# Kernel optimization log

Measured on AMD Instinct MI355X. Metric: run time of the kernel, lower is better.

The kernel has to match this reference:

```python
import jax, jax.numpy as jnp
import numpy as np

DT = 0.01
STEPS = 30
D = 2048


def setup_inputs() -> dict:
    key = jax.random.key(0)
    ks = jax.random.split(key, 7)
    B, S = 4, 4096
    x = jax.random.normal(ks[0], (B, S, D), jnp.float32)
    lorenz = jnp.array([10.0, 28.0, 8.0 / 3.0], jnp.float32)
    strength = jnp.float32(0.3)
    W_in = jax.random.normal(ks[1], (3, D), jnp.float32) / np.sqrt(D)
    b_in = jax.random.normal(ks[2], (3,), jnp.float32) * 0.01
    W_out = jax.random.normal(ks[3], (D, 18), jnp.float32) / np.sqrt(18.0)
    b_out = jax.random.normal(ks[4], (D,), jnp.float32) * 0.01
    return {"x": x, "lorenz": lorenz, "strength": strength,
            "W_in": W_in, "b_in": b_in, "W_out": W_out, "b_out": b_out}


def _deriv(s, sigma, rho, beta):
    xx, yy, zz = s[..., 0], s[..., 1], s[..., 2]
    return jnp.stack([sigma * (yy - xx), xx * (rho - zz) - yy, xx * yy - beta * zz], axis=-1)


def reference(x, lorenz, strength, W_in, b_in, W_out, b_out):
    orig_shape = x.shape
    xf = x.reshape(-1, x.shape[-1])            # [N, D]
    state0 = xf @ W_in.T + b_in                # [N, 3]
    params = jnp.clip(jnp.abs(lorenz), 0.1, None)
    sigma, rho, beta = params[0], params[1], params[2]

    def step(s, _):
        k1 = _deriv(s, sigma, rho, beta)
        k2 = _deriv(s + 0.5 * DT * k1, sigma, rho, beta)
        k3 = _deriv(s + 0.5 * DT * k2, sigma, rho, beta)
        k4 = _deriv(s + DT * k3, sigma, rho, beta)
        s2 = s + (DT / 6.0) * (k1 + 2.0 * k2 + 2.0 * k3 + k4)
        return s2, s2

    _, ys = jax.lax.scan(step, state0, None, length=STEPS)  # [STEPS, N, 3]
    traj = jnp.concatenate([state0[:, None], jnp.moveaxis(ys, 0, 1)], axis=1)  # [N, STEPS+1, 3]

    feats = jnp.concatenate([
        traj[:, 0],                         # initial state
        traj[:, -1],                        # final state
        traj.mean(axis=1),
        traj.std(axis=1, ddof=1),           # torch.std is unbiased by default
        traj.min(axis=1),
        traj.max(axis=1),
    ], axis=-1)                             # [N, 18]

    pert = feats @ W_out.T + b_out          # [N, D]
    out = xf + jnp.tanh(pert) * jnp.abs(strength)
    return out.reshape(orig_shape)
```

## Files before the change

### kernel.cpp

```cpp
#include <hip/hip_runtime.h>
#include <math.h>

#define DD 2048
#define DTC 0.01f
#define NSTEPS 30

__device__ __forceinline__ void lorenz_deriv(float x, float y, float z,
                                             float sigma, float rho, float beta,
                                             float& dx, float& dy, float& dz) {
    dx = sigma * (y - x);
    dy = x * (rho - z) - y;
    dz = x * y - beta * z;
}

__device__ __forceinline__ float fast_tanh(float p) {
    float e = __expf(2.0f * p);
    return 1.0f - __fdividef(2.0f, e + 1.0f);
}

__global__ __launch_bounds__(256) void k1_feats(
    const float* __restrict__ x, const float* __restrict__ lorenz,
    const float* __restrict__ W_in, const float* __restrict__ b_in,
    float* __restrict__ feats) {
    const int tid = threadIdx.x;
    const int row0 = blockIdx.x * 8;
    const int d0 = tid * 8;

    float w0[8], w1[8], w2[8];
    {
        const float4* p0 = reinterpret_cast<const float4*>(W_in + 0 * DD + d0);
        const float4* p1 = reinterpret_cast<const float4*>(W_in + 1 * DD + d0);
        const float4* p2 = reinterpret_cast<const float4*>(W_in + 2 * DD + d0);
        float4 a, b;
        a = p0[0]; b = p0[1];
        w0[0]=a.x; w0[1]=a.y; w0[2]=a.z; w0[3]=a.w; w0[4]=b.x; w0[5]=b.y; w0[6]=b.z; w0[7]=b.w;
        a = p1[0]; b = p1[1];
        w1[0]=a.x; w1[1]=a.y; w1[2]=a.z; w1[3]=a.w; w1[4]=b.x; w1[5]=b.y; w1[6]=b.z; w1[7]=b.w;
        a = p2[0]; b = p2[1];
        w2[0]=a.x; w2[1]=a.y; w2[2]=a.z; w2[3]=a.w; w2[4]=b.x; w2[5]=b.y; w2[6]=b.z; w2[7]=b.w;
    }

    float part[8][3];
#pragma unroll
    for (int r = 0; r < 8; ++r) {
        const float4* p = reinterpret_cast<const float4*>(x + (size_t)(row0 + r) * DD + d0);
        float4 a = p[0], b = p[1];
        float xv[8] = {a.x, a.y, a.z, a.w, b.x, b.y, b.z, b.w};
        float s0 = 0.f, s1 = 0.f, s2 = 0.f;
#pragma unroll
        for (int j = 0; j < 8; ++j) {
            s0 += xv[j] * w0[j];
            s1 += xv[j] * w1[j];
            s2 += xv[j] * w2[j];
        }
        part[r][0] = s0; part[r][1] = s1; part[r][2] = s2;
    }

    __shared__ float red[4][24];
    __shared__ float st0[8][3];
    const int lane = tid & 63;
    const int wv = tid >> 6;
#pragma unroll
    for (int r = 0; r < 8; ++r) {
#pragma unroll
        for (int k = 0; k < 3; ++k) {
            float v = part[r][k];
#pragma unroll
            for (int off = 32; off > 0; off >>= 1) v += __shfl_xor(v, off, 64);
            if (lane == 0) red[wv][r * 3 + k] = v;
        }
    }
    __syncthreads();
    if (tid < 24) {
        float v = red[0][tid] + red[1][tid] + red[2][tid] + red[3][tid] + b_in[tid % 3];
        st0[tid / 3][tid % 3] = v;
    }
    __syncthreads();

    if (tid < 8) {
        const float sigma = fmaxf(fabsf(lorenz[0]), 0.1f);
        const float rho   = fmaxf(fabsf(lorenz[1]), 0.1f);
        const float beta  = fmaxf(fabsf(lorenz[2]), 0.1f);
        float sx = st0[tid][0], sy = st0[tid][1], sz = st0[tid][2];
        const float ix = sx, iy = sy, iz = sz;
        float sux = sx, suy = sy, suz = sz;
        float sqx = sx * sx, sqy = sy * sy, sqz = sz * sz;
        float mnx = sx, mny = sy, mnz = sz;
        float mxx = sx, mxy = sy, mxz = sz;
#pragma unroll 1
        for (int t = 0; t < NSTEPS; ++t) {
            float k1x, k1y, k1z, k2x, k2y, k2z, k3x, k3y, k3z, k4x, k4y, k4z;
            float ax, ay, az;
            lorenz_deriv(sx, sy, sz, sigma, rho, beta, k1x, k1y, k1z);
            ax = sx + 0.5f * DTC * k1x; ay = sy + 0.5f * DTC * k1y; az = sz + 0.5f * DTC * k1z;
            lorenz_deriv(ax, ay, az, sigma, rho, beta, k2x, k2y, k2z);
            ax = sx + 0.5f * DTC * k2x; ay = sy + 0.5f * DTC * k2y; az = sz + 0.5f * DTC * k2z;
            lorenz_deriv(ax, ay, az, sigma, rho, beta, k3x, k3y, k3z);
            ax = sx + DTC * k3x; ay = sy + DTC * k3y; az = sz + DTC * k3z;
            lorenz_deriv(ax, ay, az, sigma, rho, beta, k4x, k4y, k4z);
            sx += (DTC / 6.0f) * (k1x + 2.0f * k2x + 2.0f * k3x + k4x);
            sy += (DTC / 6.0f) * (k1y + 2.0f * k2y + 2.0f * k3y + k4y);
            sz += (DTC / 6.0f) * (k1z + 2.0f * k2z + 2.0f * k3z + k4z);
            sux += sx; suy += sy; suz += sz;
            sqx += sx * sx; sqy += sy * sy; sqz += sz * sz;
            mnx = fminf(mnx, sx); mny = fminf(mny, sy); mnz = fminf(mnz, sz);
            mxx = fmaxf(mxx, sx); mxy = fmaxf(mxy, sy); mxz = fmaxf(mxz, sz);
        }
        const float inv31 = 1.0f / 31.0f;
        const float inv30 = 1.0f / 30.0f;
        const float mex = sux * inv31, mey = suy * inv31, mez = suz * inv31;
        const float vax = fmaxf((sqx - sux * mex) * inv30, 0.0f);
        const float vay = fmaxf((sqy - suy * mey) * inv30, 0.0f);
        const float vaz = fmaxf((sqz - suz * mez) * inv30, 0.0f);
        float* f = feats + (size_t)(row0 + tid) * 18;
        f[0]  = ix;  f[1]  = iy;  f[2]  = iz;
        f[3]  = sx;  f[4]  = sy;  f[5]  = sz;
        f[6]  = mex; f[7]  = mey; f[8]  = mez;
        f[9]  = sqrtf(vax); f[10] = sqrtf(vay); f[11] = sqrtf(vaz);
        f[12] = mnx; f[13] = mny; f[14] = mnz;
        f[15] = mxx; f[16] = mxy; f[17] = mxz;
    }
}

__global__ __launch_bounds__(256) void k2_out(
    const float* __restrict__ x, const float* __restrict__ feats,
    const float* __restrict__ W_out, const float* __restrict__ b_out,
    const float* __restrict__ strength, float* __restrict__ out) {
    const int tid = threadIdx.x;
    const int row0 = blockIdx.x * 32;
    const int j0 = blockIdx.y * 512 + tid * 2;

    float w0[18], w1[18];
    {
        const float* wp = W_out + (size_t)j0 * 18;
#pragma unroll
        for (int k = 0; k < 18; ++k) { w0[k] = wp[k]; w1[k] = wp[18 + k]; }
    }
    const float2 bo = *reinterpret_cast<const float2*>(b_out + j0);
    const float sabs = fabsf(strength[0]);

#pragma unroll 1
    for (int r = 0; r < 32; ++r) {
        const int row = row0 + r;
        const float* f = feats + (size_t)row * 18;
        float p0 = bo.x, p1 = bo.y;
#pragma unroll
        for (int k = 0; k < 18; ++k) {
            const float fk = f[k];
            p0 += fk * w0[k];
            p1 += fk * w1[k];
        }
        const float2 xv = *reinterpret_cast<const float2*>(x + (size_t)row * DD + j0);
        float2 o;
        o.x = xv.x + fast_tanh(p0) * sabs;
        o.y = xv.y + fast_tanh(p1) * sabs;
        *reinterpret_cast<float2*>(out + (size_t)row * DD + j0) = o;
    }
}

extern "C" void kernel_launch(void* const* d_in, const int* in_sizes, int n_in,
                              void* d_out, int out_size, void* d_ws, size_t ws_size,
                              hipStream_t stream) {
    const float* x        = (const float*)d_in[0];
    const float* lorenz   = (const float*)d_in[1];
    const float* strength = (const float*)d_in[2];
    const float* W_in     = (const float*)d_in[3];
    const float* b_in     = (const float*)d_in[4];
    const float* W_out    = (const float*)d_in[5];
    const float* b_out    = (const float*)d_in[6];
    float* out   = (float*)d_out;
    float* feats = (float*)d_ws;

    const int N = in_sizes[0] / DD;

    k1_feats<<<N / 8, 256, 0, stream>>>(x, lorenz, W_in, b_in, feats);

    dim3 g2(N / 32, DD / 512);
    k2_out<<<g2, 256, 0, stream>>>(x, feats, W_out, b_out, strength, out);
}
```

Baseline: 87.03 us.

## Fuse feature and output kernels with x tile staged in LDS

Merges the two kernels into one that loads a 4-row tile of x into LDS with global_load_lds, computes the projection, the RK4 trajectory and the features, then produces the output rows from the same LDS tile. This avoids reading x twice from HBM, the feats round trip through global memory, and the second launch. In exchange each block uses 32KB of LDS, which limits occupancy. W_out is now reloaded per block (2048x18 floats) with a strided, uncoalesced access, and the serial 30-step RK4 runs on only 4 threads while the rest of the block waits.

```diff
diff --git a/kernel.cpp b/kernel.cpp
--- a/kernel.cpp
+++ b/kernel.cpp
@@ -4,6 +4,7 @@
 #define DD 2048
 #define DTC 0.01f
 #define NSTEPS 30
+#define ROWS 4
 
 __device__ __forceinline__ void lorenz_deriv(float x, float y, float z,
                                              float sigma, float rho, float beta,
@@ -18,12 +19,20 @@
     return 1.0f - __fdividef(2.0f, e + 1.0f);
 }
 
-__global__ __launch_bounds__(256) void k1_feats(
+__global__ __launch_bounds__(256) void fused_enrich(
     const float* __restrict__ x, const float* __restrict__ lorenz,
     const float* __restrict__ W_in, const float* __restrict__ b_in,
-    float* __restrict__ feats) {
+    const float* __restrict__ W_out, const float* __restrict__ b_out,
+    const float* __restrict__ strength, float* __restrict__ out) {
+    __shared__ float x_tile[ROWS * DD];
+    __shared__ float red[4][ROWS * 3];
+    __shared__ float st0[ROWS][3];
+    __shared__ float feats_lds[ROWS][20];
+
     const int tid = threadIdx.x;
-    const int row0 = blockIdx.x * 8;
+    const int lane = tid & 63;
+    const int wv = tid >> 6;
+    const int row0 = blockIdx.x * ROWS;
     const int d0 = tid * 8;
 
     float w0[8], w1[8], w2[8];
@@ -40,10 +49,23 @@
         w2[0]=a.x; w2[1]=a.y; w2[2]=a.z; w2[3]=a.w; w2[4]=b.x; w2[5]=b.y; w2[6]=b.z; w2[7]=b.w;
     }
 
-    float part[8][3];
+    {
+        const float* gbase = x + (size_t)row0 * DD;
 #pragma unroll
-    for (int r = 0; r < 8; ++r) {
-        const float4* p = reinterpret_cast<const float4*>(x + (size_t)(row0 + r) * DD + d0);
+        for (int i = 0; i < 8; ++i) {
+            const int foff = wv * 2048 + i * 256;
+            __builtin_amdgcn_global_load_lds(
+                (const __attribute__((address_space(1))) unsigned int*)(gbase + foff + lane * 4),
+                (__attribute__((address_space(3))) unsigned int*)(x_tile + foff),
+                16, 0, 0);
+        }
+    }
+    __syncthreads();
+
+    float part[ROWS][3];
+#pragma unroll
+    for (int r = 0; r < ROWS; ++r) {
+        const float4* p = reinterpret_cast<const float4*>(x_tile + r * DD + d0);
         float4 a = p[0], b = p[1];
         float xv[8] = {a.x, a.y, a.z, a.w, b.x, b.y, b.z, b.w};
         float s0 = 0.f, s1 = 0.f, s2 = 0.f;
@@ -56,12 +78,8 @@
         part[r][0] = s0; part[r][1] = s1; part[r][2] = s2;
     }
 
-    __shared__ float red[4][24];
-    __shared__ float st0[8][3];
-    const int lane = tid & 63;
-    const int wv = tid >> 6;
 #pragma unroll
-    for (int r = 0; r < 8; ++r) {
+    for (int r = 0; r < ROWS; ++r) {
 #pragma unroll
         for (int k = 0; k < 3; ++k) {
             float v = part[r][k];
@@ -71,13 +89,13 @@
         }
     }
     __syncthreads();
-    if (tid < 24) {
+    if (tid < ROWS * 3) {
         float v = red[0][tid] + red[1][tid] + red[2][tid] + red[3][tid] + b_in[tid % 3];
         st0[tid / 3][tid % 3] = v;
     }
     __syncthreads();
 
-    if (tid < 8) {
+    if (tid < ROWS) {
         const float sigma = fmaxf(fabsf(lorenz[0]), 0.1f);
         const float rho   = fmaxf(fabsf(lorenz[1]), 0.1f);
         const float beta  = fmaxf(fabsf(lorenz[2]), 0.1f);
@@ -112,7 +130,7 @@
         const float vax = fmaxf((sqx - sux * mex) * inv30, 0.0f);
         const float vay = fmaxf((sqy - suy * mey) * inv30, 0.0f);
         const float vaz = fmaxf((sqz - suz * mez) * inv30, 0.0f);
-        float* f = feats + (size_t)(row0 + tid) * 18;
+        float* f = feats_lds[tid];
         f[0]  = ix;  f[1]  = iy;  f[2]  = iz;
         f[3]  = sx;  f[4]  = sy;  f[5]  = sz;
         f[6]  = mex; f[7]  = mey; f[8]  = mez;
@@ -120,41 +138,33 @@
         f[12] = mnx; f[13] = mny; f[14] = mnz;
         f[15] = mxx; f[16] = mxy; f[17] = mxz;
     }
-}
+    __syncthreads();
 
-__global__ __launch_bounds__(256) void k2_out(
-    const float* __restrict__ x, const float* __restrict__ feats,
-    const float* __restrict__ W_out, const float* __restrict__ b_out,
-    const float* __restrict__ strength, float* __restrict__ out) {
-    const int tid = threadIdx.x;
-    const int row0 = blockIdx.x * 32;
-    const int j0 = blockIdx.y * 512 + tid * 2;
+    float f[ROWS][18];
+#pragma unroll
+    for (int r = 0; r < ROWS; ++r)
+#pragma unroll
+        for (int k = 0; k < 18; ++k) f[r][k] = feats_lds[r][k];
 
-    float w0[18], w1[18];
-    {
-        const float* wp = W_out + (size_t)j0 * 18;
+    const float sabs = fabsf(strength[0]);
+#pragma unroll 1
+    for (int j = 0; j < 8; ++j) {
+        const int c = tid + j * 256;
+        float w[18];
+        {
+            const float2* wp2 = reinterpret_cast<const float2*>(W_out + (size_t)c * 18);
 #pragma unroll
-        for (int k = 0; k < 18; ++k) { w0[k] = wp[k]; w1[k] = wp[18 + k]; }
-    }
-    const float2 bo = *reinterpret_cast<const float2*>(b_out + j0);
-    const float sabs = fabsf(strength[0]);
-
-#pragma unroll 1
-    for (int r = 0; r < 32; ++r) {
-        const int row = row0 + r;
-        const float* f = feats + (size_t)row * 18;
-        float p0 = bo.x, p1 = bo.y;
+            for (int k = 0; k < 9; ++k) { float2 t = wp2[k]; w[2*k] = t.x; w[2*k+1] = t.y; }
+        }
+        const float bo = b_out[c];
 #pragma unroll
-        for (int k = 0; k < 18; ++k) {
-            const float fk = f[k];
-            p0 += fk * w0[k];
-            p1 += fk * w1[k];
+        for (int r = 0; r < ROWS; ++r) {
+            float p = bo;
+#pragma unroll
+            for (int k = 0; k < 18; ++k) p += f[r][k] * w[k];
+            const float xv = x_tile[r * DD + c];
+            out[(size_t)(row0 + r) * DD + c] = xv + fast_tanh(p) * sabs;
         }
-        const float2 xv = *reinterpret_cast<const float2*>(x + (size_t)row * DD + j0);
-        float2 o;
-        o.x = xv.x + fast_tanh(p0) * sabs;
-        o.y = xv.y + fast_tanh(p1) * sabs;
-        *reinterpret_cast<float2*>(out + (size_t)row * DD + j0) = o;
     }
 }
 
@@ -168,13 +178,10 @@
     const float* b_in     = (const float*)d_in[4];
     const float* W_out    = (const float*)d_in[5];
     const float* b_out    = (const float*)d_in[6];
-    float* out   = (float*)d_out;
-    float* feats = (float*)d_ws;
+    float* out = (float*)d_out;
 
     const int N = in_sizes[0] / DD;
 
-    k1_feats<<<N / 8, 256, 0, stream>>>(x, lorenz, W_in, b_in, feats);
-
-    dim3 g2(N / 32, DD / 512);
-    k2_out<<<g2, 256, 0, stream>>>(x, feats, W_out, b_out, strength, out);
+    fused_enrich<<<N / ROWS, 256, 0, stream>>>(
+        x, lorenz, W_in, b_in, W_out, b_out, strength, out);
 }
```

Result: no change. 88.09 us (+1.2%).

## Split Lorenz integration into its own fully parallel kernel and widen output tiles

Applied to the files above, without the earlier changes.

The old first kernel ran the 30-step RK4 integration on only 8 of 256 threads per block after the projection, which left most lanes idle on a serial chain. The projection now runs in its own kernel with half-wave-per-row reductions and no shared memory. A separate kernel integrates one row per thread across all lanes. The output kernel processes 4 columns and 2 rows per thread and uses nontemporal stores. This adds an extra launch and a small state0 round-trip through memory.

```diff
diff --git a/kernel.cpp b/kernel.cpp
--- a/kernel.cpp
+++ b/kernel.cpp
@@ -4,6 +4,8 @@
 #define DD 2048
 #define DTC 0.01f
 #define NSTEPS 30
+
+typedef float floatx4 __attribute__((ext_vector_type(4)));
 
 __device__ __forceinline__ void lorenz_deriv(float x, float y, float z,
                                              float sigma, float rho, float beta,
@@ -18,143 +20,140 @@
     return 1.0f - __fdividef(2.0f, e + 1.0f);
 }
 
-__global__ __launch_bounds__(256) void k1_feats(
-    const float* __restrict__ x, const float* __restrict__ lorenz,
-    const float* __restrict__ W_in, const float* __restrict__ b_in,
-    float* __restrict__ feats) {
+__global__ __launch_bounds__(256) void kA_state0(
+    const float* __restrict__ x, const float* __restrict__ W_in,
+    const float* __restrict__ b_in, float* __restrict__ state0) {
     const int tid = threadIdx.x;
-    const int row0 = blockIdx.x * 8;
-    const int d0 = tid * 8;
+    const int lane = tid & 63;
+    const int half = lane >> 5;
+    const int wv = tid >> 6;
+    const int row = blockIdx.x * 8 + wv * 2 + half;
+    const int c0 = (lane & 31) * 64;
 
-    float w0[8], w1[8], w2[8];
-    {
-        const float4* p0 = reinterpret_cast<const float4*>(W_in + 0 * DD + d0);
-        const float4* p1 = reinterpret_cast<const float4*>(W_in + 1 * DD + d0);
-        const float4* p2 = reinterpret_cast<const float4*>(W_in + 2 * DD + d0);
-        float4 a, b;
-        a = p0[0]; b = p0[1];
-        w0[0]=a.x; w0[1]=a.y; w0[2]=a.z; w0[3]=a.w; w0[4]=b.x; w0[5]=b.y; w0[6]=b.z; w0[7]=b.w;
-        a = p1[0]; b = p1[1];
-        w1[0]=a.x; w1[1]=a.y; w1[2]=a.z; w1[3]=a.w; w1[4]=b.x; w1[5]=b.y; w1[6]=b.z; w1[7]=b.w;
-        a = p2[0]; b = p2[1];
-        w2[0]=a.x; w2[1]=a.y; w2[2]=a.z; w2[3]=a.w; w2[4]=b.x; w2[5]=b.y; w2[6]=b.z; w2[7]=b.w;
+    const float* xp  = x + (size_t)row * DD + c0;
+    const float* w0p = W_in + 0 * DD + c0;
+    const float* w1p = W_in + 1 * DD + c0;
+    const float* w2p = W_in + 2 * DD + c0;
+
+    floatx4 a0 = {0.f,0.f,0.f,0.f}, a1 = a0, a2 = a0;
+#pragma unroll
+    for (int i = 0; i < 16; ++i) {
+        const floatx4 xv = *reinterpret_cast<const floatx4*>(xp + 4 * i);
+        a0 += xv * *reinterpret_cast<const floatx4*>(w0p + 4 * i);
+        a1 += xv * *reinterpret_cast<const floatx4*>(w1p + 4 * i);
+        a2 += xv * *reinterpret_cast<const floatx4*>(w2p + 4 * i);
     }
-
-    float part[8][3];
+    float s0 = a0.x + a0.y + a0.z + a0.w;
+    float s1 = a1.x + a1.y + a1.z + a1.w;
+    float s2 = a2.x + a2.y + a2.z + a2.w;
 #pragma unroll
-    for (int r = 0; r < 8; ++r) {
-        const float4* p = reinterpret_cast<const float4*>(x + (size_t)(row0 + r) * DD + d0);
-        float4 a = p[0], b = p[1];
-        float xv[8] = {a.x, a.y, a.z, a.w, b.x, b.y, b.z, b.w};
-        float s0 = 0.f, s1 = 0.f, s2 = 0.f;
-#pragma unroll
-        for (int j = 0; j < 8; ++j) {
-            s0 += xv[j] * w0[j];
-            s1 += xv[j] * w1[j];
-            s2 += xv[j] * w2[j];
-        }
-        part[r][0] = s0; part[r][1] = s1; part[r][2] = s2;
+    for (int off = 16; off > 0; off >>= 1) {
+        s0 += __shfl_xor(s0, off, 64);
+        s1 += __shfl_xor(s1, off, 64);
+        s2 += __shfl_xor(s2, off, 64);
     }
-
-    __shared__ float red[4][24];
-    __shared__ float st0[8][3];
-    const int lane = tid & 63;
-    const int wv = tid >> 6;
-#pragma unroll
-    for (int r = 0; r < 8; ++r) {
-#pragma unroll
-        for (int k = 0; k < 3; ++k) {
-            float v = part[r][k];
-#pragma unroll
-            for (int off = 32; off > 0; off >>= 1) v += __shfl_xor(v, off, 64);
-            if (lane == 0) red[wv][r * 3 + k] = v;
-        }
-    }
-    __syncthreads();
-    if (tid < 24) {
-        float v = red[0][tid] + red[1][tid] + red[2][tid] + red[3][tid] + b_in[tid % 3];
-        st0[tid / 3][tid % 3] = v;
-    }
-    __syncthreads();
-
-    if (tid < 8) {
-        const float sigma = fmaxf(fabsf(lorenz[0]), 0.1f);
-        const float rho   = fmaxf(fabsf(lorenz[1]), 0.1f);
-        const float beta  = fmaxf(fabsf(lorenz[2]), 0.1f);
-        float sx = st0[tid][0], sy = st0[tid][1], sz = st0[tid][2];
-        const float ix = sx, iy = sy, iz = sz;
-        float sux = sx, suy = sy, suz = sz;
-        float sqx = sx * sx, sqy = sy * sy, sqz = sz * sz;
-        float mnx = sx, mny = sy, mnz = sz;
-        float mxx = sx, mxy = sy, mxz = sz;
-#pragma unroll 1
-        for (int t = 0; t < NSTEPS; ++t) {
-            float k1x, k1y, k1z, k2x, k2y, k2z, k3x, k3y, k3z, k4x, k4y, k4z;
-            float ax, ay, az;
-            lorenz_deriv(sx, sy, sz, sigma, rho, beta, k1x, k1y, k1z);
-            ax = sx + 0.5f * DTC * k1x; ay = sy + 0.5f * DTC * k1y; az = sz + 0.5f * DTC * k1z;
-            lorenz_deriv(ax, ay, az, sigma, rho, beta, k2x, k2y, k2z);
-            ax = sx + 0.5f * DTC * k2x; ay = sy + 0.5f * DTC * k2y; az = sz + 0.5f * DTC * k2z;
-            lorenz_deriv(ax, ay, az, sigma, rho, beta, k3x, k3y, k3z);
-            ax = sx + DTC * k3x; ay = sy + DTC * k3y; az = sz + DTC * k3z;
-            lorenz_deriv(ax, ay, az, sigma, rho, beta, k4x, k4y, k4z);
-            sx += (DTC / 6.0f) * (k1x + 2.0f * k2x + 2.0f * k3x + k4x);
-            sy += (DTC / 6.0f) * (k1y + 2.0f * k2y + 2.0f * k3y + k4y);
-            sz += (DTC / 6.0f) * (k1z + 2.0f * k2z + 2.0f * k3z + k4z);
-            sux += sx; suy += sy; suz += sz;
-            sqx += sx * sx; sqy += sy * sy; sqz += sz * sz;
-            mnx = fminf(mnx, sx); mny = fminf(mny, sy); mnz = fminf(mnz, sz);
-            mxx = fmaxf(mxx, sx); mxy = fmaxf(mxy, sy); mxz = fmaxf(mxz, sz);
-        }
-        const float inv31 = 1.0f / 31.0f;
-        const float inv30 = 1.0f / 30.0f;
-        const float mex = sux * inv31, mey = suy * inv31, mez = suz * inv31;
-        const float vax = fmaxf((sqx - sux * mex) * inv30, 0.0f);
-        const float vay = fmaxf((sqy - suy * mey) * inv30, 0.0f);
-        const float vaz = fmaxf((sqz - suz * mez) * inv30, 0.0f);
-        float* f = feats + (size_t)(row0 + tid) * 18;
-        f[0]  = ix;  f[1]  = iy;  f[2]  = iz;
-        f[3]  = sx;  f[4]  = sy;  f[5]  = sz;
-        f[6]  = mex; f[7]  = mey; f[8]  = mez;
-        f[9]  = sqrtf(vax); f[10] = sqrtf(vay); f[11] = sqrtf(vaz);
-        f[12] = mnx; f[13] = mny; f[14] = mnz;
-        f[15] = mxx; f[16] = mxy; f[17] = mxz;
+    if ((lane & 31) == 0) {
+        float* sp = state0 + (size_t)row * 3;
+        sp[0] = s0 + b_in[0];
+        sp[1] = s1 + b_in[1];
+        sp[2] = s2 + b_in[2];
     }
 }
 
-__global__ __launch_bounds__(256) void k2_out(
+__global__ __launch_bounds__(256) void kB_integrate(
+    const float* __restrict__ state0, const float* __restrict__ lorenz,
+    float* __restrict__ feats) {
+    const int row = blockIdx.x * 256 + threadIdx.x;
+    const float sigma = fmaxf(fabsf(lorenz[0]), 0.1f);
+    const float rho   = fmaxf(fabsf(lorenz[1]), 0.1f);
+    const float beta  = fmaxf(fabsf(lorenz[2]), 0.1f);
+
+    float sx = state0[(size_t)row * 3 + 0];
+    float sy = state0[(size_t)row * 3 + 1];
+    float sz = state0[(size_t)row * 3 + 2];
+    const float ix = sx, iy = sy, iz = sz;
+    float sux = sx, suy = sy, suz = sz;
+    float sqx = sx * sx, sqy = sy * sy, sqz = sz * sz;
+    float mnx = sx, mny = sy, mnz = sz;
+    float mxx = sx, mxy = sy, mxz = sz;
+#pragma unroll 1
+    for (int t = 0; t < NSTEPS; ++t) {
+        float k1x, k1y, k1z, k2x, k2y, k2z, k3x, k3y, k3z, k4x, k4y, k4z;
+        float ax, ay, az;
+        lorenz_deriv(sx, sy, sz, sigma, rho, beta, k1x, k1y, k1z);
+        ax = sx + 0.5f * DTC * k1x; ay = sy + 0.5f * DTC * k1y; az = sz + 0.5f * DTC * k1z;
+        lorenz_deriv(ax, ay, az, sigma, rho, beta, k2x, k2y, k2z);
+        ax = sx + 0.5f * DTC * k2x; ay = sy + 0.5f * DTC * k2y; az = sz + 0.5f * DTC * k2z;
+        lorenz_deriv(ax, ay, az, sigma, rho, beta, k3x, k3y, k3z);
+        ax = sx + DTC * k3x; ay = sy + DTC * k3y; az = sz + DTC * k3z;
+        lorenz_deriv(ax, ay, az, sigma, rho, beta, k4x, k4y, k4z);
+        sx += (DTC / 6.0f) * (k1x + 2.0f * k2x + 2.0f * k3x + k4x);
+        sy += (DTC / 6.0f) * (k1y + 2.0f * k2y + 2.0f * k3y + k4y);
+        sz += (DTC / 6.0f) * (k1z + 2.0f * k2z + 2.0f * k3z + k4z);
+        sux += sx; suy += sy; suz += sz;
+        sqx += sx * sx; sqy += sy * sy; sqz += sz * sz;
+        mnx = fminf(mnx, sx); mny = fminf(mny, sy); mnz = fminf(mnz, sz);
+        mxx = fmaxf(mxx, sx); mxy = fmaxf(mxy, sy); mxz = fmaxf(mxz, sz);
+    }
+    const float inv31 = 1.0f / 31.0f;
+    const float inv30 = 1.0f / 30.0f;
+    const float mex = sux * inv31, mey = suy * inv31, mez = suz * inv31;
+    const float vax = fmaxf((sqx - sux * mex) * inv30, 0.0f);
+    const float vay = fmaxf((sqy - suy * mey) * inv30, 0.0f);
+    const float vaz = fmaxf((sqz - suz * mez) * inv30, 0.0f);
+    float* f = feats + (size_t)row * 18;
+    f[0]  = ix;  f[1]  = iy;  f[2]  = iz;
+    f[3]  = sx;  f[4]  = sy;  f[5]  = sz;
+    f[6]  = mex; f[7]  = mey; f[8]  = mez;
+    f[9]  = sqrtf(vax); f[10] = sqrtf(vay); f[11] = sqrtf(vaz);
+    f[12] = mnx; f[13] = mny; f[14] = mnz;
+    f[15] = mxx; f[16] = mxy; f[17] = mxz;
+}
+
+__global__ __launch_bounds__(256) void kC_out(
     const float* __restrict__ x, const float* __restrict__ feats,
     const float* __restrict__ W_out, const float* __restrict__ b_out,
     const float* __restrict__ strength, float* __restrict__ out) {
     const int tid = threadIdx.x;
     const int row0 = blockIdx.x * 32;
-    const int j0 = blockIdx.y * 512 + tid * 2;
+    const int c0 = blockIdx.y * 1024 + tid * 4;
 
-    float w0[18], w1[18];
-    {
-        const float* wp = W_out + (size_t)j0 * 18;
+    float w[4][18];
 #pragma unroll
-        for (int k = 0; k < 18; ++k) { w0[k] = wp[k]; w1[k] = wp[18 + k]; }
+    for (int cc = 0; cc < 4; ++cc) {
+        const float2* wp2 = reinterpret_cast<const float2*>(W_out + (size_t)(c0 + cc) * 18);
+#pragma unroll
+        for (int k = 0; k < 9; ++k) { float2 t = wp2[k]; w[cc][2*k] = t.x; w[cc][2*k+1] = t.y; }
     }
-    const float2 bo = *reinterpret_cast<const float2*>(b_out + j0);
+    const floatx4 bo = *reinterpret_cast<const floatx4*>(b_out + c0);
     const float sabs = fabsf(strength[0]);
 
 #pragma unroll 1
-    for (int r = 0; r < 32; ++r) {
-        const int row = row0 + r;
-        const float* f = feats + (size_t)row * 18;
-        float p0 = bo.x, p1 = bo.y;
+    for (int r = 0; r < 32; r += 2) {
+        const int rowA = row0 + r, rowB = row0 + r + 1;
+        const float* fA = feats + (size_t)rowA * 18;
+        const float* fB = feats + (size_t)rowB * 18;
+        const floatx4 xA = *reinterpret_cast<const floatx4*>(x + (size_t)rowA * DD + c0);
+        const floatx4 xB = *reinterpret_cast<const floatx4*>(x + (size_t)rowB * DD + c0);
+        floatx4 pA = bo, pB = bo;
 #pragma unroll
         for (int k = 0; k < 18; ++k) {
-            const float fk = f[k];
-            p0 += fk * w0[k];
-            p1 += fk * w1[k];
+            const float fa = fA[k], fb = fB[k];
+            const floatx4 wk = { w[0][k], w[1][k], w[2][k], w[3][k] };
+            pA += fa * wk;
+            pB += fb * wk;
         }
-        const float2 xv = *reinterpret_cast<const float2*>(x + (size_t)row * DD + j0);
-        float2 o;
-        o.x = xv.x + fast_tanh(p0) * sabs;
-        o.y = xv.y + fast_tanh(p1) * sabs;
-        *reinterpret_cast<float2*>(out + (size_t)row * DD + j0) = o;
+        floatx4 oA, oB;
+        oA.x = xA.x + fast_tanh(pA.x) * sabs;
+        oA.y = xA.y + fast_tanh(pA.y) * sabs;
+        oA.z = xA.z + fast_tanh(pA.z) * sabs;
+        oA.w = xA.w + fast_tanh(pA.w) * sabs;
+        oB.x = xB.x + fast_tanh(pB.x) * sabs;
+        oB.y = xB.y + fast_tanh(pB.y) * sabs;
+        oB.z = xB.z + fast_tanh(pB.z) * sabs;
+        oB.w = xB.w + fast_tanh(pB.w) * sabs;
+        __builtin_nontemporal_store(oA, reinterpret_cast<floatx4*>(out + (size_t)rowA * DD + c0));
+        __builtin_nontemporal_store(oB, reinterpret_cast<floatx4*>(out + (size_t)rowB * DD + c0));
     }
 }
 
@@ -168,13 +167,14 @@
     const float* b_in     = (const float*)d_in[4];
     const float* W_out    = (const float*)d_in[5];
     const float* b_out    = (const float*)d_in[6];
-    float* out   = (float*)d_out;
-    float* feats = (float*)d_ws;
+    float* out = (float*)d_out;
 
     const int N = in_sizes[0] / DD;
+    float* state0 = (float*)d_ws;
+    float* feats  = state0 + (size_t)N * 3;
 
-    k1_feats<<<N / 8, 256, 0, stream>>>(x, lorenz, W_in, b_in, feats);
-
-    dim3 g2(N / 32, DD / 512);
-    k2_out<<<g2, 256, 0, stream>>>(x, feats, W_out, b_out, strength, out);
+    kA_state0<<<N / 8, 256, 0, stream>>>(x, W_in, b_in, state0);
+    kB_integrate<<<N / 256, 256, 0, stream>>>(state0, lorenz, feats);
+    dim3 g3(N / 32, DD / 1024);
+    kC_out<<<g3, 256, 0, stream>>>(x, feats, W_out, b_out, strength, out);
 }
```

After: 127.5 us. +46.5%, slower.
